# Kernel optimization log

Hardware: AMD Instinct MI355X
Metric: run time of the kernel (lower is better)

## Reference

```python
import jax, jax.numpy as jnp
import numpy as np
import math

NVX = 4096   # vx grid points -> th, vr_vxvy are [NVX, NVX]
NVR = 256    # radial grid points
NL = 2       # max spherical-harmonic degree (original hardcodes n_max=2)
N_LM = (NL + 1) * (NL + 2) // 2  # number of (l, m) pairs with 0<=m<=l<=NL


def _grids():
    vmax_x = 8.0
    dvx = 2.0 * vmax_x / NVX
    vx = jnp.linspace(-vmax_x + dvx / 2, vmax_x - dvx / 2, NVX)
    vmax_r = 8.0 * 1.05 * math.sqrt(2.0)
    dvr = vmax_r / NVR
    vr = jnp.linspace(dvr / 2, vmax_r - dvr / 2, NVR)
    VX, VY = jnp.meshgrid(vx, vx)
    th = jnp.arctan2(VY, VX)
    vr_vxvy = jnp.sqrt(VX ** 2 + VY ** 2)
    return vr.astype(jnp.float32), th.astype(jnp.float32), vr_vxvy.astype(jnp.float32)


def _assoc_legendre(l, m, x):
    """P_l^m(x) with Condon-Shortley phase (matches scipy/jax sph_harm)."""
    pmm = jnp.ones_like(x)
    if m > 0:
        somx2 = jnp.sqrt((1.0 - x) * (1.0 + x))
        fact = 1.0
        for _ in range(m):
            pmm = pmm * (-fact) * somx2
            fact += 2.0
    if l == m:
        return pmm
    pmmp1 = x * (2.0 * m + 1.0) * pmm
    if l == m + 1:
        return pmmp1
    for ll in range(m + 2, l + 1):
        pll = ((2.0 * ll - 1.0) * x * pmmp1 - (ll + m - 1.0) * pmm) / (ll - m)
        pmm, pmmp1 = pmmp1, pll
    return pmmp1


def _ylm_real_theta0(l, m, costh):
    # Re[Y_l^m(theta=0, phi)] = K_lm * P_l^m(cos phi); exp(i*m*0) = 1
    k = math.sqrt((2 * l + 1) / (4.0 * math.pi)
                  * math.factorial(l - m) / math.factorial(l + m))
    return k * _assoc_legendre(l, m, costh)


def setup_inputs() -> dict:
    key = jax.random.key(0)
    # flm stacked row-major over (l, m): (0,0),(1,0),(1,1),(2,0),(2,1),(2,2)
    flm = jax.random.uniform(key, (N_LM, NVR), dtype=jnp.float32)
    vr, th, vr_vxvy = _grids()
    return {"flm": flm, "vr": vr, "th": th, "vr_vxvy": vr_vxvy}


def reference(flm, vr, th, vr_vxvy):
    costh = jnp.cos(th)
    fvxvy = jnp.zeros_like(vr_vxvy)
    idx = 0
    for l in range(NL + 1):
        for m in range(l + 1):
            # gather-based 1D interpolation of radial coefficient onto 2D grid
            f_r = jnp.interp(vr_vxvy, vr, flm[idx], right=1e-16)
            y_lm = _ylm_real_theta0(l, m, costh)
            fvxvy = fvxvy + f_r * y_lm
            idx += 1
    return fvxvy
```

## Files before the change

### kernel.cpp

```cpp
#include <hip/hip_runtime.h>


__global__ __launch_bounds__(256) void sph_eval_kernel(
    const float* __restrict__ flm,
    const float* __restrict__ vr,
    float* __restrict__ out)
{
    __shared__ float2 P[6 * 256];

    const int t = threadIdx.x;

    {
        const float C[6] = {
            0.28209479177387814f,
            0.48860251190291992f,
           -0.34549414947133547f,
            0.63078313050504010f,
           -0.77254840404650040f,
            0.38627420202325020f };
        const int k = t;
        #pragma unroll
        for (int i = 0; i < 6; ++i) {
            const float f0 = flm[i * 256 + k];
            const float f1 = flm[i * 256 + (k < 255 ? k + 1 : 255)];
            P[i * 256 + k] = make_float2(C[i] * f0, C[i] * f1);
        }
    }
    __syncthreads();

    const float dvx = 16.0f / 4096.0f;
    const float vx0 = -8.0f + 0.5f * dvx;

    const float vr0     = vr[0];
    const float inv_dvr = 1.0f / (vr[1] - vr0);

    #pragma unroll
    for (int rr = 0; rr < 2; ++rr) {
        const int row = blockIdx.x * 2 + rr;
        const float vxi  = fmaf((float)row, dvx, vx0);
        const float avxi = fabsf(vxi);
        const float vxi2 = vxi * vxi;
        const size_t r0 = (size_t)row * 4096;
        const size_t r1 = (size_t)(4095 - row) * 4096;

        #pragma unroll
        for (int qq = 0; qq < 2; ++qq) {
            const int j0 = qq * 1024 + t * 4;

            float ev[4], od[4];
            #pragma unroll
            for (int q = 0; q < 4; ++q) {
                const float vxj  = fmaf((float)(j0 + q), dvx, vx0);
                const float rsq  = fmaf(vxj, vxj, vxi2);
                const float rinv = __builtin_amdgcn_rsqf(rsq);
                const float r    = rsq * rinv;
                const float x    = vxj  * rinv;
                const float s    = avxi * rinv;

                float tt = (r - vr0) * inv_dvr;
                tt = fminf(fmaxf(tt, 0.0f), 254.999f);
                const float kf = floorf(tt);
                const float w  = tt - kf;
                const int   k  = (int)kf;

                const float2 p0 = P[k];
                const float2 p1 = P[256 + k];
                const float2 p2 = P[512 + k];
                const float2 p3 = P[768 + k];
                const float2 p4 = P[1024 + k];
                const float2 p5 = P[1280 + k];

                const float g0 = fmaf(w, p0.y - p0.x, p0.x);
                const float g1 = fmaf(w, p1.y - p1.x, p1.x);
                const float g2 = fmaf(w, p2.y - p2.x, p2.x);
                const float g3 = fmaf(w, p3.y - p3.x, p3.x);
                const float g4 = fmaf(w, p4.y - p4.x, p4.x);
                const float g5 = fmaf(w, p5.y - p5.x, p5.x);

                const float xx = x * x;
                float e = g0;
                e = fmaf(g2, s, e);
                e = fmaf(g3, fmaf(1.5f, xx, -0.5f), e);
                e = fmaf(g5, s * s, e);
                const float o = fmaf(g4, x * s, g1 * x);
                ev[q] = e;
                od[q] = o;
            }

            const float4 oa = { ev[0] + od[0], ev[1] + od[1],
                                ev[2] + od[2], ev[3] + od[3] };
            const float4 ob = { ev[3] - od[3], ev[2] - od[2],
                                ev[1] - od[1], ev[0] - od[0] };

            *reinterpret_cast<float4*>(out + r0 + j0)          = oa;
            *reinterpret_cast<float4*>(out + r0 + (4092 - j0)) = ob;
            *reinterpret_cast<float4*>(out + r1 + j0)          = oa;
            *reinterpret_cast<float4*>(out + r1 + (4092 - j0)) = ob;
        }
    }
}

extern "C" void kernel_launch(void* const* d_in, const int* in_sizes, int n_in,
                              void* d_out, int out_size, void* d_ws, size_t ws_size,
                              hipStream_t stream) {
    const float* flm = (const float*)d_in[0];
    const float* vr  = (const float*)d_in[1];
    float* out = (float*)d_out;

    sph_eval_kernel<<<dim3(1024), 256, 0, stream>>>(flm, vr, out);
}
```

Before: 18.17 us.

## Stage row in LDS for coalesced stores, one row per block, precompute slopes

Each block now computes a single row, writes it into a shared-memory row buffer, then stores it to both mirrored output rows with fully contiguous float4 writes. The reversed-half stores that previously went straight to global now go through LDS, and the grid doubles to 2048 blocks. The interpolation table stores slopes instead of next values, the index clamp uses one fma and drops the upper clamp, and the odd term is refactored to save a multiply. The cost is an extra LDS round trip plus a barrier, more LDS per block, and the table fill repeated in twice as many blocks.

Measured after the change: 18.67 us. +2.8%, slower.

```diff
diff --git a/kernel.cpp b/kernel.cpp
--- a/kernel.cpp
+++ b/kernel.cpp
@@ -7,6 +7,7 @@
     float* __restrict__ out)
 {
     __shared__ float2 P[6 * 256];
+    __shared__ float  rowbuf[4096];
 
     const int t = threadIdx.x;
 
@@ -23,7 +24,7 @@
         for (int i = 0; i < 6; ++i) {
             const float f0 = flm[i * 256 + k];
             const float f1 = flm[i * 256 + (k < 255 ? k + 1 : 255)];
-            P[i * 256 + k] = make_float2(C[i] * f0, C[i] * f1);
+            P[i * 256 + k] = make_float2(C[i] * f0, C[i] * (f1 - f0));
         }
     }
     __syncthreads();
@@ -33,70 +34,74 @@
 
     const float vr0     = vr[0];
     const float inv_dvr = 1.0f / (vr[1] - vr0);
+    const float c0      = -vr0 * inv_dvr;
+
+    const int row = blockIdx.x;
+    const float vxi  = fmaf((float)row, dvx, vx0);
+    const float avxi = fabsf(vxi);
+    const float vxi2 = vxi * vxi;
 
     #pragma unroll
-    for (int rr = 0; rr < 2; ++rr) {
-        const int row = blockIdx.x * 2 + rr;
-        const float vxi  = fmaf((float)row, dvx, vx0);
-        const float avxi = fabsf(vxi);
-        const float vxi2 = vxi * vxi;
-        const size_t r0 = (size_t)row * 4096;
-        const size_t r1 = (size_t)(4095 - row) * 4096;
+    for (int qq = 0; qq < 2; ++qq) {
+        const int j0 = qq * 1024 + t * 4;
 
+        float ev[4], od[4];
         #pragma unroll
-        for (int qq = 0; qq < 2; ++qq) {
-            const int j0 = qq * 1024 + t * 4;
+        for (int q = 0; q < 4; ++q) {
+            const float vxj  = fmaf((float)(j0 + q), dvx, vx0);
+            const float rsq  = fmaf(vxj, vxj, vxi2);
+            const float rinv = __builtin_amdgcn_rsqf(rsq);
+            const float r    = rsq * rinv;
+            const float x    = vxj  * rinv;
+            const float s    = avxi * rinv;
 
-            float ev[4], od[4];
-            #pragma unroll
-            for (int q = 0; q < 4; ++q) {
-                const float vxj  = fmaf((float)(j0 + q), dvx, vx0);
-                const float rsq  = fmaf(vxj, vxj, vxi2);
-                const float rinv = __builtin_amdgcn_rsqf(rsq);
-                const float r    = rsq * rinv;
-                const float x    = vxj  * rinv;
-                const float s    = avxi * rinv;
+            float tt = fmaxf(fmaf(r, inv_dvr, c0), 0.0f);
+            const float kf = floorf(tt);
+            const float w  = tt - kf;
+            const int   k  = (int)kf;
 
-                float tt = (r - vr0) * inv_dvr;
-                tt = fminf(fmaxf(tt, 0.0f), 254.999f);
-                const float kf = floorf(tt);
-                const float w  = tt - kf;
-                const int   k  = (int)kf;
+            const float2 p0 = P[k];
+            const float2 p1 = P[256 + k];
+            const float2 p2 = P[512 + k];
+            const float2 p3 = P[768 + k];
+            const float2 p4 = P[1024 + k];
+            const float2 p5 = P[1280 + k];
 
-                const float2 p0 = P[k];
-                const float2 p1 = P[256 + k];
-                const float2 p2 = P[512 + k];
-                const float2 p3 = P[768 + k];
-                const float2 p4 = P[1024 + k];
-                const float2 p5 = P[1280 + k];
+            const float g0 = fmaf(w, p0.y, p0.x);
+            const float g1 = fmaf(w, p1.y, p1.x);
+            const float g2 = fmaf(w, p2.y, p2.x);
+            const float g3 = fmaf(w, p3.y, p3.x);
+            const float g4 = fmaf(w, p4.y, p4.x);
+            const float g5 = fmaf(w, p5.y, p5.x);
 
-                const float g0 = fmaf(w, p0.y - p0.x, p0.x);
-                const float g1 = fmaf(w, p1.y - p1.x, p1.x);
-                const float g2 = fmaf(w, p2.y - p2.x, p2.x);
-                const float g3 = fmaf(w, p3.y - p3.x, p3.x);
-                const float g4 = fmaf(w, p4.y - p4.x, p4.x);
-                const float g5 = fmaf(w, p5.y - p5.x, p5.x);
+            const float xx = x * x;
+            float e = g0;
+            e = fmaf(g2, s, e);
+            e = fmaf(g3, fmaf(1.5f, xx, -0.5f), e);
+            e = fmaf(g5, s * s, e);
+            const float o = x * fmaf(g4, s, g1);
+            ev[q] = e;
+            od[q] = o;
+        }
 
-                const float xx = x * x;
-                float e = g0;
-                e = fmaf(g2, s, e);
-                e = fmaf(g3, fmaf(1.5f, xx, -0.5f), e);
-                e = fmaf(g5, s * s, e);
-                const float o = fmaf(g4, x * s, g1 * x);
-                ev[q] = e;
-                od[q] = o;
-            }
+        const float4 oa = { ev[0] + od[0], ev[1] + od[1],
+                            ev[2] + od[2], ev[3] + od[3] };
+        const float4 ob = { ev[3] - od[3], ev[2] - od[2],
+                            ev[1] - od[1], ev[0] - od[0] };
 
-            const float4 oa = { ev[0] + od[0], ev[1] + od[1],
-                                ev[2] + od[2], ev[3] + od[3] };
-            const float4 ob = { ev[3] - od[3], ev[2] - od[2],
-                                ev[1] - od[1], ev[0] - od[0] };
+        *reinterpret_cast<float4*>(&rowbuf[j0])        = oa;
+        *reinterpret_cast<float4*>(&rowbuf[4092 - j0]) = ob;
+    }
+    __syncthreads();
 
-            *reinterpret_cast<float4*>(out + r0 + j0)          = oa;
-            *reinterpret_cast<float4*>(out + r0 + (4092 - j0)) = ob;
-            *reinterpret_cast<float4*>(out + r1 + j0)          = oa;
-            *reinterpret_cast<float4*>(out + r1 + (4092 - j0)) = ob;
-        }
+    const size_t r0 = (size_t)row * 4096;
+    const size_t r1 = (size_t)(4095 - row) * 4096;
+    #pragma unroll
+    for (int p = 0; p < 4; ++p) {
+        const int idx = p * 1024 + t * 4;
+        const float4 v = *reinterpret_cast<const float4*>(&rowbuf[idx]);
+        *reinterpret_cast<float4*>(out + r0 + idx) = v;
+        *reinterpret_cast<float4*>(out + r1 + idx) = v;
     }
 }
 
@@ -107,5 +112,5 @@
     const float* vr  = (const float*)d_in[1];
     float* out = (float*)d_out;
 
-    sph_eval_kernel<<<dim3(1024), 256, 0, stream>>>(flm, vr, out);
+    sph_eval_kernel<<<dim3(2048), 256, 0, stream>>>(flm, vr, out);
 }
```

## Fold Legendre terms into five coefficient tables and halve rows per block

Applied to the files above, without the earlier changes.

Uses x^2 = 1 - s^2 to fold the P20 term into the constant and s^2 coefficients. This leaves five precombined tables instead of six, and each table stores the value plus its forward difference, so each interpolation is a single FMA. It also drops the upper clamp, folds the vr0 offset into an FMA, and launches 2048 blocks with one row each instead of 1024 blocks with two rows. The aim is fewer LDS reads and ALU ops per output, at the cost of redoing the table setup in twice as many blocks.

Result: no change. 17.84 us (-1.8%).

```diff
diff --git a/kernel.cpp b/kernel.cpp
--- a/kernel.cpp
+++ b/kernel.cpp
@@ -6,25 +6,41 @@
     const float* __restrict__ vr,
     float* __restrict__ out)
 {
-    __shared__ float2 P[6 * 256];
+    __shared__ float2 P[5 * 256];
 
     const int t = threadIdx.x;
 
     {
-        const float C[6] = {
-            0.28209479177387814f,
-            0.48860251190291992f,
-           -0.34549414947133547f,
-            0.63078313050504010f,
-           -0.77254840404650040f,
-            0.38627420202325020f };
-        const int k = t;
-        #pragma unroll
-        for (int i = 0; i < 6; ++i) {
-            const float f0 = flm[i * 256 + k];
-            const float f1 = flm[i * 256 + (k < 255 ? k + 1 : 255)];
-            P[i * 256 + k] = make_float2(C[i] * f0, C[i] * f1);
-        }
+        const float C0 = 0.28209479177387814f;
+        const float C1 = 0.48860251190291992f;
+        const float C2 = -0.34549414947133547f;
+        const float C3 = 0.63078313050504010f;
+        const float C4 = -0.77254840404650040f;
+        const float C5 = 0.38627420202325020f;
+
+        const int k  = t;
+        const int k1 = (k < 255) ? k + 1 : 255;
+
+        const float f00 = flm[0 * 256 + k], f00n = flm[0 * 256 + k1];
+        const float f10 = flm[1 * 256 + k], f10n = flm[1 * 256 + k1];
+        const float f11 = flm[2 * 256 + k], f11n = flm[2 * 256 + k1];
+        const float f20 = flm[3 * 256 + k], f20n = flm[3 * 256 + k1];
+        const float f21 = flm[4 * 256 + k], f21n = flm[4 * 256 + k1];
+        const float f22 = flm[5 * 256 + k], f22n = flm[5 * 256 + k1];
+
+        const float a0 = fmaf(C0, f00, C3 * f20);
+        const float a1 = fmaf(C0, f00n, C3 * f20n);
+        const float b0 = C2 * f11,  b1 = C2 * f11n;
+        const float c0 = fmaf(C5, f22, -1.5f * C3 * f20);
+        const float c1 = fmaf(C5, f22n, -1.5f * C3 * f20n);
+        const float d0 = C1 * f10,  d1 = C1 * f10n;
+        const float e0 = C4 * f21,  e1 = C4 * f21n;
+
+        P[          k] = make_float2(a0, a1 - a0);
+        P[ 256 +    k] = make_float2(b0, b1 - b0);
+        P[ 512 +    k] = make_float2(c0, c1 - c0);
+        P[ 768 +    k] = make_float2(d0, d1 - d0);
+        P[1024 +    k] = make_float2(e0, e1 - e0);
     }
     __syncthreads();
 
@@ -33,70 +49,59 @@
 
     const float vr0     = vr[0];
     const float inv_dvr = 1.0f / (vr[1] - vr0);
+    const float cc0     = -vr0 * inv_dvr;
+
+    const int row = blockIdx.x;
+    const float vxi  = fmaf((float)row, dvx, vx0);
+    const float avxi = fabsf(vxi);
+    const float vxi2 = vxi * vxi;
+    const size_t r0 = (size_t)row * 4096;
+    const size_t r1 = (size_t)(4095 - row) * 4096;
 
     #pragma unroll
-    for (int rr = 0; rr < 2; ++rr) {
-        const int row = blockIdx.x * 2 + rr;
-        const float vxi  = fmaf((float)row, dvx, vx0);
-        const float avxi = fabsf(vxi);
-        const float vxi2 = vxi * vxi;
-        const size_t r0 = (size_t)row * 4096;
-        const size_t r1 = (size_t)(4095 - row) * 4096;
+    for (int qq = 0; qq < 2; ++qq) {
+        const int j0 = qq * 1024 + t * 4;
 
+        float ev[4], od[4];
         #pragma unroll
-        for (int qq = 0; qq < 2; ++qq) {
-            const int j0 = qq * 1024 + t * 4;
+        for (int q = 0; q < 4; ++q) {
+            const float vxj  = fmaf((float)(j0 + q), dvx, vx0);
+            const float rsq  = fmaf(vxj, vxj, vxi2);
+            const float rinv = __builtin_amdgcn_rsqf(rsq);
+            const float r    = rsq * rinv;
+            const float x    = vxj  * rinv;
+            const float s    = avxi * rinv;
 
-            float ev[4], od[4];
-            #pragma unroll
-            for (int q = 0; q < 4; ++q) {
-                const float vxj  = fmaf((float)(j0 + q), dvx, vx0);
-                const float rsq  = fmaf(vxj, vxj, vxi2);
-                const float rinv = __builtin_amdgcn_rsqf(rsq);
-                const float r    = rsq * rinv;
-                const float x    = vxj  * rinv;
-                const float s    = avxi * rinv;
+            float tt = fmaxf(fmaf(r, inv_dvr, cc0), 0.0f);
+            const float kf = floorf(tt);
+            const float w  = tt - kf;
+            const int   k  = (int)kf;
 
-                float tt = (r - vr0) * inv_dvr;
-                tt = fminf(fmaxf(tt, 0.0f), 254.999f);
-                const float kf = floorf(tt);
-                const float w  = tt - kf;
-                const int   k  = (int)kf;
+            const float2 pA = P[k];
+            const float2 pB = P[256 + k];
+            const float2 pC = P[512 + k];
+            const float2 pD = P[768 + k];
+            const float2 pE = P[1024 + k];
 
-                const float2 p0 = P[k];
-                const float2 p1 = P[256 + k];
-                const float2 p2 = P[512 + k];
-                const float2 p3 = P[768 + k];
-                const float2 p4 = P[1024 + k];
-                const float2 p5 = P[1280 + k];
+            const float gA = fmaf(w, pA.y, pA.x);
+            const float gB = fmaf(w, pB.y, pB.x);
+            const float gC = fmaf(w, pC.y, pC.x);
+            const float gD = fmaf(w, pD.y, pD.x);
+            const float gE = fmaf(w, pE.y, pE.x);
 
-                const float g0 = fmaf(w, p0.y - p0.x, p0.x);
-                const float g1 = fmaf(w, p1.y - p1.x, p1.x);
-                const float g2 = fmaf(w, p2.y - p2.x, p2.x);
-                const float g3 = fmaf(w, p3.y - p3.x, p3.x);
-                const float g4 = fmaf(w, p4.y - p4.x, p4.x);
-                const float g5 = fmaf(w, p5.y - p5.x, p5.x);
+            ev[q] = fmaf(s, fmaf(s, gC, gB), gA);
+            od[q] = x * fmaf(s, gE, gD);
+        }
 
-                const float xx = x * x;
-                float e = g0;
-                e = fmaf(g2, s, e);
-                e = fmaf(g3, fmaf(1.5f, xx, -0.5f), e);
-                e = fmaf(g5, s * s, e);
-                const float o = fmaf(g4, x * s, g1 * x);
-                ev[q] = e;
-                od[q] = o;
-            }
+        const float4 oa = { ev[0] + od[0], ev[1] + od[1],
+                            ev[2] + od[2], ev[3] + od[3] };
+        const float4 ob = { ev[3] - od[3], ev[2] - od[2],
+                            ev[1] - od[1], ev[0] - od[0] };
 
-            const float4 oa = { ev[0] + od[0], ev[1] + od[1],
-                                ev[2] + od[2], ev[3] + od[3] };
-            const float4 ob = { ev[3] - od[3], ev[2] - od[2],
-                                ev[1] - od[1], ev[0] - od[0] };
-
-            *reinterpret_cast<float4*>(out + r0 + j0)          = oa;
-            *reinterpret_cast<float4*>(out + r0 + (4092 - j0)) = ob;
-            *reinterpret_cast<float4*>(out + r1 + j0)          = oa;
-            *reinterpret_cast<float4*>(out + r1 + (4092 - j0)) = ob;
-        }
+        *reinterpret_cast<float4*>(out + r0 + j0)          = oa;
+        *reinterpret_cast<float4*>(out + r0 + (4092 - j0)) = ob;
+        *reinterpret_cast<float4*>(out + r1 + j0)          = oa;
+        *reinterpret_cast<float4*>(out + r1 + (4092 - j0)) = ob;
     }
 }
 
@@ -107,5 +112,5 @@
     const float* vr  = (const float*)d_in[1];
     float* out = (float*)d_out;
 
-    sph_eval_kernel<<<dim3(1024), 256, 0, stream>>>(flm, vr, out);
+    sph_eval_kernel<<<dim3(2048), 256, 0, stream>>>(flm, vr, out);
 }
```
